# Kernel tuning notes

Measured on AMD Instinct MI355X. Metric: run time of the kernel, lower is better.

The kernel has to match this reference:

```python
import jax, jax.numpy as jnp
import numpy as np

B = 32768   # batch of states (original forward is per-state; we vmap)
D = 3       # coord_dim

_W_SHAPES = [("w_h0",(3,32)),("w_y0",(3,32)),("w_yu0",(3,3)),("w_u0",(3,32)),
             ("w_h1",(32,32)),("w_z1",(32,32)),("w_zu1",(32,32)),("w_y1",(3,32)),
             ("w_yu1",(32,3)),("w_u1",(32,32)),("w_h2",(32,32)),("w_z2",(32,32)),
             ("w_zu2",(32,32)),("w_y2",(3,32)),("w_yu2",(32,3)),("w_u2",(32,32)),
             ("w_z_out",(32,1)),("w_zu_out",(32,32)),("w_y_out",(3,1)),
             ("w_yu_out",(32,3)),("w_u_out",(32,1))]
_B_SHAPES = [("b_y0",(3,)),("b_h0",(32,)),("b_0",(32,)),("b_h1",(32,)),("b_y1",(3,)),
             ("b_z1",(32,)),("b_1",(32,)),("b_h2",(32,)),("b_z2",(32,)),("b_y2",(3,)),
             ("b_2",(32,)),("b_z_out",(32,)),("b_y_out",(3,)),("b_out",(1,))]

def _make_params(key):
    n = len(_W_SHAPES) + len(_B_SHAPES) + 4
    ks = jax.random.split(key, n)
    p, i = {}, 0
    for name, sh in _W_SHAPES:   # torch .uniform_(-0.1, 0.1)
        p[name] = jax.random.uniform(ks[i], sh, jnp.float32, -0.1, 0.1); i += 1
    for name, sh in _B_SHAPES:   # torch.rand -> U[0,1)
        p[name] = jax.random.uniform(ks[i], sh, jnp.float32, 0.0, 1.0); i += 1
    # fc layers: normal init per _init_weights (stds / sqrt(16)=4), zero bias
    stds = [2.2/4.0, 0.58/4.0, 0.58*2.0/4.0, 4.0]
    shapes = [(32, 3), (32, 32), (32, 32), (1, 32)]
    for j in range(4):
        p[f"fc{j+1}_w"] = stds[j] * jax.random.normal(ks[i], shapes[j], jnp.float32); i += 1
        p[f"fc{j+1}_b"] = jnp.zeros((shapes[j][0],), jnp.float32)
    return p

def setup_inputs():
    key = jax.random.key(0)
    kx, kp = jax.random.split(key)
    inp = {"x": jax.random.normal(kx, (B, 2 * D), jnp.float32)}
    inp.update(_make_params(kp))
    return inp

def _forward(x, p):
    sp, relu = jax.nn.softplus, jax.nn.relu

    def lagr(state):
        q, y = state[:D], state[D:]
        u1 = sp(q @ p["w_h0"] + p["b_h0"])
        z1 = sp((y * (q @ p["w_yu0"] + p["b_y0"])) @ p["w_y0"] + q @ p["w_u0"] + p["b_0"])
        u2 = sp(u1 @ p["w_h1"] + p["b_h1"])
        z2 = sp((z1 * (u1 @ p["w_zu1"] + p["b_z1"])) @ relu(p["w_z1"])
                + (y * (u1 @ p["w_yu1"] + p["b_y1"])) @ p["w_y1"]
                + u1 @ p["w_u1"] + p["b_1"])
        u3 = sp(u2 @ p["w_h2"] + p["b_h2"])
        z3 = sp((z2 * (u2 @ p["w_zu2"] + p["b_z2"])) @ relu(p["w_z2"])
                + (y * (u2 @ p["w_yu2"] + p["b_y2"])) @ p["w_y2"]
                + u2 @ p["w_u2"] + p["b_2"])
        zout = sp((z3 * (u3 @ p["w_zu_out"] + p["b_z_out"])) @ relu(p["w_z_out"])
                  + (y * (u3 @ p["w_yu_out"] + p["b_y_out"])) @ p["w_y_out"]
                  + u3 @ p["w_u_out"] + p["b_out"])
        V = sp(q @ p["fc1_w"].T + p["fc1_b"])
        V = sp(V @ p["fc2_w"].T + p["fc2_b"])
        V = sp(V @ p["fc3_w"].T + p["fc3_b"])
        V = V @ p["fc4_w"].T + p["fc4_b"]
        return (zout - V)[0]  # scalar Lagrangian

    def step(state):
        dq = state[D:]
        H = jax.hessian(lagr)(state)        # (6,6)
        g = jax.grad(lagr)(state)[:D]       # dL/dq, matches jacobian row b[0,:3]
        M = H[D:, D:]                       # d2L/ddq ddq
        C = H[D:, :D]                       # d2L/ddq dq
        ddq = (g - dq @ C.T) @ jnp.linalg.inv(M).T
        dx = jnp.concatenate([dq, ddq])
        return state + 0.001 * dx           # Euler step, as in torch forward

    return jax.vmap(step)(x)

def reference(x, w_h0, w_y0, w_yu0, w_u0, w_h1, w_z1, w_zu1, w_y1, w_yu1, w_u1,
              w_h2, w_z2, w_zu2, w_y2, w_yu2, w_u2, w_z_out, w_zu_out, w_y_out,
              w_yu_out, w_u_out, b_y0, b_h0, b_0, b_h1, b_y1, b_z1, b_1, b_h2,
              b_z2, b_y2, b_2, b_z_out, b_y_out, b_out, fc1_w, fc1_b, fc2_w,
              fc2_b, fc3_w, fc3_b, fc4_w, fc4_b):
    p = dict(locals())
    xv = p.pop("x")
    return _forward(xv, p)
```

## Files before the change

### kernel.cpp

```cpp
#include <hip/hip_runtime.h>

#define NTH 64
#define B_TOTAL 32768
#define PSTR 20

typedef float v2f __attribute__((ext_vector_type(2)));
typedef float v4f __attribute__((ext_vector_type(4)));
typedef double v4d __attribute__((ext_vector_type(4)));

struct Ptrs { const float* p[44]; };

enum : int {
  I_X = 0,
  I_WH0 = 1, I_WY0 = 2, I_WYU0 = 3, I_WU0 = 4,
  I_WH1 = 5, I_WZ1 = 6, I_WZU1 = 7, I_WY1 = 8, I_WYU1 = 9, I_WU1 = 10,
  I_WH2 = 11, I_WZ2 = 12, I_WZU2 = 13, I_WY2 = 14, I_WYU2 = 15, I_WU2 = 16,
  I_WZO = 17, I_WZUO = 18, I_WYO = 19, I_WYUO = 20, I_WUO = 21,
  I_BY0 = 22, I_BH0 = 23, I_B0 = 24, I_BH1 = 25, I_BY1 = 26, I_BZ1 = 27, I_B1 = 28,
  I_BH2 = 29, I_BZ2 = 30, I_BY2 = 31, I_B2 = 32, I_BZO = 33, I_BYO = 34, I_BOUT = 35,
  I_FC1 = 36, I_FC1B = 37, I_FC2 = 38, I_FC2B = 39, I_FC3 = 40, I_FC3B = 41,
  I_FC4 = 42, I_FC4B = 43
};

struct V16 { float c[16]; };

__device__ __forceinline__ float spf(float x) {
  return fmaxf(x, 0.0f) + __logf(1.0f + __expf(-fabsf(x)));
}
__device__ __forceinline__ float sigf(float x) {
  return __fdividef(1.0f, 1.0f + __expf(-x));
}

__device__ __forceinline__ V16 spchain16(const V16& A, float y0, float y1, float y2) {
  V16 Z;
  float s = sigf(A.c[0]);
  float d = s * (1.0f - s);
  Z.c[0] = spf(A.c[0]);
#pragma unroll
  for (int a = 0; a < 3; ++a) Z.c[1 + a] = s * A.c[1 + a];
#pragma unroll
  for (int b = 0; b < 3; ++b) Z.c[4 + b] = s * A.c[4 + b];
  Z.c[7]  = s * A.c[7]  + d * A.c[1] * A.c[1];
  Z.c[8]  = s * A.c[8]  + d * A.c[1] * A.c[2];
  Z.c[9]  = s * A.c[9]  + d * A.c[1] * A.c[3];
  Z.c[10] = s * A.c[10] + d * A.c[2] * A.c[2];
  Z.c[11] = s * A.c[11] + d * A.c[2] * A.c[3];
  Z.c[12] = s * A.c[12] + d * A.c[3] * A.c[3];
  float ydq = y0 * A.c[4] + y1 * A.c[5] + y2 * A.c[6];
#pragma unroll
  for (int a = 0; a < 3; ++a) Z.c[13 + a] = s * A.c[13 + a] + d * A.c[1 + a] * ydq;
  return Z;
}

__device__ __forceinline__ void stageProd(float* row, const V16& Z, float S0, float S1,
                                          float S2, float S3, float y0, float y1, float y2) {
  float z0 = Z.c[0];
  float ysd = y0 * S1 + y1 * S2 + y2 * S3;
  v4f w0 = {z0 * S0, S0 * Z.c[1], S0 * Z.c[2], S0 * Z.c[3]};
  v4f w1 = {z0 * S1 + S0 * Z.c[4], z0 * S2 + S0 * Z.c[5], z0 * S3 + S0 * Z.c[6], S0 * Z.c[7]};
  v4f w2 = {S0 * Z.c[8], S0 * Z.c[9], S0 * Z.c[10], S0 * Z.c[11]};
  v4f w3 = {S0 * Z.c[12], S0 * Z.c[13] + Z.c[1] * ysd, S0 * Z.c[14] + Z.c[2] * ysd,
            S0 * Z.c[15] + Z.c[3] * ysd};
  *(v4f*)(row + 0) = w0;  *(v4f*)(row + 4) = w1;
  *(v4f*)(row + 8) = w2;  *(v4f*)(row + 12) = w3;
}

__device__ __forceinline__ V16 prodZS16(const V16& Z, float S0, float S1, float S2, float S3,
                                        float y0, float y1, float y2) {
  V16 P;
  const float Sq[3] = {S1, S2, S3};
  float ysd = y0 * S1 + y1 * S2 + y2 * S3;
  P.c[0] = Z.c[0] * S0;
#pragma unroll
  for (int a = 0; a < 3; ++a) P.c[1 + a] = S0 * Z.c[1 + a];
#pragma unroll
  for (int b = 0; b < 3; ++b) P.c[4 + b] = Z.c[0] * Sq[b] + S0 * Z.c[4 + b];
#pragma unroll
  for (int t = 0; t < 6; ++t) P.c[7 + t] = S0 * Z.c[7 + t];
#pragma unroll
  for (int a = 0; a < 3; ++a) P.c[13 + a] = S0 * Z.c[13 + a] + Z.c[1 + a] * ysd;
  return P;
}

__device__ __forceinline__ void stageU_all(const float* __restrict__ Wh,
                                           const float* __restrict__ Wzu,
                                           const float* __restrict__ Wu,
                                           const float* __restrict__ Wyu, int j,
                                           const float* us,
                                           v2f& h0, v2f& h1, v2f& s0, v2f& s1,
                                           v2f& w0, v2f& w1,
                                           v2f& ta0, v2f& ta1, v2f& tb0, v2f& tb1,
                                           v2f& tc0, v2f& tc1) {
#pragma unroll 2
  for (int i = 0; i < 32; ++i) {
    v4f u = *(const v4f*)(us + i * 4);
    float wh = Wh[i * 32 + j], wz = Wzu[i * 32 + j], wu = Wu[i * 32 + j];
    h0 += u.xy * wh; h1 += u.zw * wh;
    s0 += u.xy * wz; s1 += u.zw * wz;
    w0 += u.xy * wu; w1 += u.zw * wu;
    float wy0 = Wyu[i * 3 + 0], wy1 = Wyu[i * 3 + 1], wy2 = Wyu[i * 3 + 2];
    ta0 += u.xy * wy0; ta1 += u.zw * wy0;
    tb0 += u.xy * wy1; tb1 += u.zw * wy1;
    tc0 += u.xy * wy2; tc1 += u.zw * wy2;
  }
}

__device__ __forceinline__ void buildA16(const float* __restrict__ Wy, int j, float y0, float y1,
                                         float y2, const float wv[4], const float ta[4],
                                         const float tb[4], const float tc[4], V16& A) {
  float wy0 = Wy[j], wy1 = Wy[32 + j], wy2 = Wy[64 + j];
  A.c[0] = wv[0] + y0 * ta[0] * wy0 + y1 * tb[0] * wy1 + y2 * tc[0] * wy2;
  A.c[1] = ta[0] * wy0; A.c[2] = tb[0] * wy1; A.c[3] = tc[0] * wy2;
#pragma unroll
  for (int b = 0; b < 3; ++b)
    A.c[4 + b] = wv[1 + b] + y0 * ta[1 + b] * wy0 + y1 * tb[1 + b] * wy1 + y2 * tc[1 + b] * wy2;
#pragma unroll
  for (int t6 = 0; t6 < 6; ++t6) A.c[7 + t6] = 0.0f;
  float yta = y0 * ta[1] + y1 * ta[2] + y2 * ta[3];
  float ytb = y0 * tb[1] + y1 * tb[2] + y2 * tb[3];
  float ytc = y0 * tc[1] + y1 * tc[2] + y2 * tc[3];
  A.c[13] = yta * wy0; A.c[14] = ytb * wy1; A.c[15] = ytc * wy2;
}

__global__ __launch_bounds__(NTH, 4) void lnn_step_kernel(Ptrs P, float* __restrict__ out) {
  __shared__ float pstage[2][32][PSTR];
  __shared__ float ustage[2][32][4];

  const int tid = threadIdx.x;
  const int j = tid & 31;
  const int half = tid >> 5;
  const int sample = blockIdx.x * 2 + half;

  float* prow = &pstage[half][0][0];
  float* urow = &ustage[half][0][0];
  float* pst0 = &pstage[0][0][0];
  float* pst1 = &pstage[1][0][0];
  const int l64 = tid & 63;
  const int n16 = l64 & 15;
  const int kq = l64 >> 4;

  const float* X = P.p[I_X] + sample * 6;
  const float q0 = X[0], q1 = X[1], q2 = X[2];
  const float y0 = X[3], y1 = X[4], y2 = X[5];

  float Vg0, Vg1, Vg2;
  {
    const float* fc1 = P.p[I_FC1];
    float f0 = fc1[j * 3], f1 = fc1[j * 3 + 1], f2 = fc1[j * 3 + 2];
    float hp = P.p[I_FC1B][j] + q0 * f0 + q1 * f1 + q2 * f2;
    float ss = sigf(hp);
    *(v4f*)(urow + j * 4) = (v4f){spf(hp), ss * f0, ss * f1, ss * f2};
    const float* fc2 = P.p[I_FC2] + j * 32;
    v2f a0 = {P.p[I_FC2B][j], 0.0f}, a1 = {0.0f, 0.0f};
#pragma unroll 2
    for (int r = 0; r < 8; ++r) {
      v4f w4 = *(const v4f*)(fc2 + r * 4);
      v4f u0 = *(const v4f*)(urow + (r * 4 + 0) * 4);
      v4f u1 = *(const v4f*)(urow + (r * 4 + 1) * 4);
      v4f u2 = *(const v4f*)(urow + (r * 4 + 2) * 4);
      v4f u3 = *(const v4f*)(urow + (r * 4 + 3) * 4);
      a0 += u0.xy * w4.x; a1 += u0.zw * w4.x;
      a0 += u1.xy * w4.y; a1 += u1.zw * w4.y;
      a0 += u2.xy * w4.z; a1 += u2.zw * w4.z;
      a0 += u3.xy * w4.w; a1 += u3.zw * w4.w;
    }
    float ss2 = sigf(a0.x);
    *(v4f*)(urow + j * 4) = (v4f){spf(a0.x), ss2 * a0.y, ss2 * a1.x, ss2 * a1.y};
    const float* fc3 = P.p[I_FC3] + j * 32;
    v2f b0 = {P.p[I_FC3B][j], 0.0f}, b1 = {0.0f, 0.0f};
#pragma unroll 2
    for (int r = 0; r < 8; ++r) {
      v4f w4 = *(const v4f*)(fc3 + r * 4);
      v4f u0 = *(const v4f*)(urow + (r * 4 + 0) * 4);
      v4f u1 = *(const v4f*)(urow + (r * 4 + 1) * 4);
      v4f u2 = *(const v4f*)(urow + (r * 4 + 2) * 4);
      v4f u3 = *(const v4f*)(urow + (r * 4 + 3) * 4);
      b0 += u0.xy * w4.x; b1 += u0.zw * w4.x;
      b0 += u1.xy * w4.y; b1 += u1.zw * w4.y;
      b0 += u2.xy * w4.z; b1 += u2.zw * w4.z;
      b0 += u3.xy * w4.w; b1 += u3.zw * w4.w;
    }
    float ss3 = sigf(b0.x);
    float f4 = P.p[I_FC4][j];
    Vg0 = ss3 * b0.y * f4; Vg1 = ss3 * b1.x * f4; Vg2 = ss3 * b1.y * f4;
  }

  const float* yu0 = P.p[I_WYU0];
  float t0v[3];
#pragma unroll
  for (int k = 0; k < 3; ++k)
    t0v[k] = q0 * yu0[k] + q1 * yu0[3 + k] + q2 * yu0[6 + k] + P.p[I_BY0][k];

  float u1c[4];
  {
    const float* wh0 = P.p[I_WH0];
    float w0 = wh0[j], w1 = wh0[32 + j], w2 = wh0[64 + j];
    float h = P.p[I_BH0][j] + q0 * w0 + q1 * w1 + q2 * w2;
    float ss = sigf(h);
    u1c[0] = spf(h); u1c[1] = ss * w0; u1c[2] = ss * w1; u1c[3] = ss * w2;
  }

  V16 z;
  {
    const float* Wy = P.p[I_WY0];
    const float* Wu = P.p[I_WU0];
    float wy0 = Wy[j], wy1 = Wy[32 + j], wy2 = Wy[64 + j];
    float wu0 = Wu[j], wu1 = Wu[32 + j], wu2 = Wu[64 + j];
    V16 A;
    A.c[0] = P.p[I_B0][j] + (y0 * t0v[0]) * wy0 + (y1 * t0v[1]) * wy1 + (y2 * t0v[2]) * wy2 +
             q0 * wu0 + q1 * wu1 + q2 * wu2;
    A.c[1] = t0v[0] * wy0; A.c[2] = t0v[1] * wy1; A.c[3] = t0v[2] * wy2;
#pragma unroll
    for (int b = 0; b < 3; ++b) {
      float acc = (b == 0 ? wu0 : (b == 1 ? wu1 : wu2));
      acc += y0 * yu0[b * 3 + 0] * wy0 + y1 * yu0[b * 3 + 1] * wy1 + y2 * yu0[b * 3 + 2] * wy2;
      A.c[4 + b] = acc;
    }
#pragma unroll
    for (int t = 0; t < 6; ++t) A.c[7 + t] = 0.0f;
    float yty0 = y0 * yu0[0] + y1 * yu0[3] + y2 * yu0[6];
    float yty1 = y0 * yu0[1] + y1 * yu0[4] + y2 * yu0[7];
    float yty2 = y0 * yu0[2] + y1 * yu0[5] + y2 * yu0[8];
    A.c[13] = yty0 * wy0; A.c[14] = yty1 * wy1; A.c[15] = yty2 * wy2;
    z = spchain16(A, y0, y1, y2);
  }

  float unext[4];
#pragma unroll 1
  for (int lvl = 0; lvl < 2; ++lvl) {
    const float* Wh  = P.p[lvl == 0 ? I_WH1 : I_WH2];
    const float* Wzu = P.p[lvl == 0 ? I_WZU1 : I_WZU2];
    const float* Wu  = P.p[lvl == 0 ? I_WU1 : I_WU2];
    const float* Wyu = P.p[lvl == 0 ? I_WYU1 : I_WYU2];
    const float* Wy  = P.p[lvl == 0 ? I_WY1 : I_WY2];
    const float* Wz  = P.p[lvl == 0 ? I_WZ1 : I_WZ2];
    const float* Bh  = P.p[lvl == 0 ? I_BH1 : I_BH2];
    const float* Bz  = P.p[lvl == 0 ? I_BZ1 : I_BZ2];
    const float* Bl  = P.p[lvl == 0 ? I_B1 : I_B2];
    const float* By  = P.p[lvl == 0 ? I_BY1 : I_BY2];

    const float* uc = (lvl == 0) ? u1c : unext;
    *(v4f*)(urow + j * 4) = (v4f){uc[0], uc[1], uc[2], uc[3]};

    v2f h0 = {Bh[j], 0.0f}, h1 = {0.0f, 0.0f};
    v2f s0 = {Bz[j], 0.0f}, s1 = {0.0f, 0.0f};
    v2f w0 = {Bl[j], 0.0f}, w1 = {0.0f, 0.0f};
    v2f ta0 = {By[0], 0.0f}, ta1 = {0.0f, 0.0f};
    v2f tb0 = {By[1], 0.0f}, tb1 = {0.0f, 0.0f};
    v2f tc0 = {By[2], 0.0f}, tc1 = {0.0f, 0.0f};
    stageU_all(Wh, Wzu, Wu, Wyu, j, urow, h0, h1, s0, s1, w0, w1,
               ta0, ta1, tb0, tb1, tc0, tc1);
    {
      float ss = sigf(h0.x);
      unext[0] = spf(h0.x); unext[1] = ss * h0.y; unext[2] = ss * h1.x; unext[3] = ss * h1.y;
    }
    stageProd(prow + j * PSTR, z, s0.x, s0.y, s1.x, s1.y, y0, y1, y2);

    v4d a00 = {0.0, 0.0, 0.0, 0.0};
    v4d a01 = {0.0, 0.0, 0.0, 0.0};
    v4d a10 = {0.0, 0.0, 0.0, 0.0};
    v4d a11 = {0.0, 0.0, 0.0, 0.0};
#pragma unroll
    for (int c = 0; c < 8; ++c) {
      const int i = c * 4 + kq;
      double b0 = (double)pst0[i * PSTR + n16];
      double b1 = (double)pst1[i * PSTR + n16];
      double wlo = (double)fmaxf(Wz[i * 32 + n16], 0.0f);
      double whi = (double)fmaxf(Wz[i * 32 + 16 + n16], 0.0f);
      a00 = __builtin_amdgcn_mfma_f64_16x16x4f64(wlo, b0, a00, 0, 0, 0);
      a01 = __builtin_amdgcn_mfma_f64_16x16x4f64(whi, b0, a01, 0, 0, 0);
      a10 = __builtin_amdgcn_mfma_f64_16x16x4f64(wlo, b1, a10, 0, 0, 0);
      a11 = __builtin_amdgcn_mfma_f64_16x16x4f64(whi, b1, a11, 0, 0, 0);
    }
#pragma unroll
    for (int r = 0; r < 4; ++r) {
      pst0[(kq + 4 * r) * PSTR + n16]        = (float)a00[r];
      pst0[(16 + kq + 4 * r) * PSTR + n16]   = (float)a01[r];
      pst1[(kq + 4 * r) * PSTR + n16]        = (float)a10[r];
      pst1[(16 + kq + 4 * r) * PSTR + n16]   = (float)a11[r];
    }

    float wvv[4] = {w0.x, w0.y, w1.x, w1.y};
    float tav[4] = {ta0.x, ta0.y, ta1.x, ta1.y};
    float tbv[4] = {tb0.x, tb0.y, tb1.x, tb1.y};
    float tcv[4] = {tc0.x, tc0.y, tc1.x, tc1.y};
    V16 A2;
    buildA16(Wy, j, y0, y1, y2, wvv, tav, tbv, tcv, A2);

    {
      const float* rown = prow + j * PSTR;
      v4f r0 = *(const v4f*)(rown + 0);
      v4f r1 = *(const v4f*)(rown + 4);
      v4f r2 = *(const v4f*)(rown + 8);
      v4f r3 = *(const v4f*)(rown + 12);
      A2.c[0] += r0.x;  A2.c[1] += r0.y;  A2.c[2] += r0.z;  A2.c[3] += r0.w;
      A2.c[4] += r1.x;  A2.c[5] += r1.y;  A2.c[6] += r1.z;  A2.c[7] += r1.w;
      A2.c[8] += r2.x;  A2.c[9] += r2.y;  A2.c[10] += r2.z; A2.c[11] += r2.w;
      A2.c[12] += r3.x; A2.c[13] += r3.y; A2.c[14] += r3.z; A2.c[15] += r3.w;
    }
    z = spchain16(A2, y0, y1, y2);
  }

  *(v4f*)(urow + j * 4) = (v4f){unext[0], unext[1], unext[2], unext[3]};
  v2f s30 = {P.p[I_BZO][j], 0.0f}, s31 = {0.0f, 0.0f};
  v2f wo0 = {0.0f, 0.0f}, wo1 = {0.0f, 0.0f};
  v2f t3a0 = {P.p[I_BYO][0], 0.0f}, t3a1 = {0.0f, 0.0f};
  v2f t3b0 = {P.p[I_BYO][1], 0.0f}, t3b1 = {0.0f, 0.0f};
  v2f t3c0 = {P.p[I_BYO][2], 0.0f}, t3c1 = {0.0f, 0.0f};
  {
    const float* Wzuo = P.p[I_WZUO];
    const float* Wuo = P.p[I_WUO];
    const float* Wyuo = P.p[I_WYUO];
#pragma unroll 2
    for (int i = 0; i < 32; ++i) {
      v4f u = *(const v4f*)(urow + i * 4);
      float wz = Wzuo[i * 32 + j];
      s30 += u.xy * wz; s31 += u.zw * wz;
      float wu = Wuo[i];
      wo0 += u.xy * wu; wo1 += u.zw * wu;
      float wy0 = Wyuo[i * 3], wy1 = Wyuo[i * 3 + 1], wy2 = Wyuo[i * 3 + 2];
      t3a0 += u.xy * wy0; t3a1 += u.zw * wy0;
      t3b0 += u.xy * wy1; t3b1 += u.zw * wy1;
      t3c0 += u.xy * wy2; t3c1 += u.zw * wy2;
    }
  }
  const float woc[4] = {wo0.x, wo0.y, wo1.x, wo1.y};
  const float t3av[4] = {t3a0.x, t3a0.y, t3a1.x, t3a1.y};
  const float t3bv[4] = {t3b0.x, t3b0.y, t3b1.x, t3b1.y};
  const float t3cv[4] = {t3c0.x, t3c0.y, t3c1.x, t3c1.y};

  float red[19];
  {
    V16 p3 = prodZS16(z, s30.x, s30.y, s31.x, s31.y, y0, y1, y2);
    float wz = fmaxf(P.p[I_WZO][j], 0.0f);
#pragma unroll
    for (int k = 0; k < 16; ++k) red[k] = p3.c[k] * wz;
    red[16] = Vg0; red[17] = Vg1; red[18] = Vg2;
  }
#pragma unroll
  for (int m = 16; m >= 1; m >>= 1) {
#pragma unroll
    for (int k = 0; k < 19; ++k) red[k] += __shfl_xor(red[k], m, 32);
  }

  if (j == 0) {
    const float* Wyo = P.p[I_WYO];
    const float wyo0 = Wyo[0], wyo1 = Wyo[1], wyo2 = Wyo[2];
    float Av = red[0] + woc[0] + P.p[I_BOUT][0] + y0 * t3av[0] * wyo0 +
               y1 * t3bv[0] * wyo1 + y2 * t3cv[0] * wyo2;
    float Agy[3];
    Agy[0] = red[1] + t3av[0] * wyo0;
    Agy[1] = red[2] + t3bv[0] * wyo1;
    Agy[2] = red[3] + t3cv[0] * wyo2;
    float Agq[3];
#pragma unroll
    for (int b = 0; b < 3; ++b)
      Agq[b] = red[4 + b] + woc[1 + b] + y0 * t3av[1 + b] * wyo0 +
               y1 * t3bv[1 + b] * wyo1 + y2 * t3cv[1 + b] * wyo2;
    float ycq[3];
    ycq[0] = red[13] + (y0 * t3av[1] + y1 * t3av[2] + y2 * t3av[3]) * wyo0;
    ycq[1] = red[14] + (y0 * t3bv[1] + y1 * t3bv[2] + y2 * t3bv[3]) * wyo1;
    ycq[2] = red[15] + (y0 * t3cv[1] + y1 * t3cv[2] + y2 * t3cv[3]) * wyo2;
    float s = sigf(Av), d = s * (1.0f - s);

    double Mm[3][3];
    const int pa[6] = {0, 0, 0, 1, 1, 2}, pb[6] = {0, 1, 2, 1, 2, 2};
#pragma unroll
    for (int t = 0; t < 6; ++t) {
      double m = (double)s * (double)red[7 + t] +
                 (double)d * (double)Agy[pa[t]] * (double)Agy[pb[t]];
      Mm[pa[t]][pb[t]] = m; Mm[pb[t]][pa[t]] = m;
    }
    double yAgq = (double)y0 * (double)Agq[0] + (double)y1 * (double)Agq[1] +
                  (double)y2 * (double)Agq[2];
    double rr[3];
#pragma unroll
    for (int a = 0; a < 3; ++a) {
      double g = (double)s * (double)Agq[a] - (double)red[16 + a];
      double Cy = (double)s * (double)ycq[a] + (double)d * (double)Agy[a] * yAgq;
      rr[a] = g - Cy;
    }
    double a = Mm[0][0], b_ = Mm[0][1], c_ = Mm[0][2], dd = Mm[1][1], e = Mm[1][2], f = Mm[2][2];
    double A00 = dd * f - e * e, A01 = c_ * e - b_ * f, A02 = b_ * e - c_ * dd;
    double A11 = a * f - c_ * c_, A12 = b_ * c_ - a * e, A22 = a * dd - b_ * b_;
    double det = a * A00 + b_ * A01 + c_ * A02;
    double idet = 1.0 / det;
    double d0 = (A00 * rr[0] + A01 * rr[1] + A02 * rr[2]) * idet;
    double d1 = (A01 * rr[0] + A11 * rr[1] + A12 * rr[2]) * idet;
    double d2 = (A02 * rr[0] + A12 * rr[1] + A22 * rr[2]) * idet;

    float* O = out + (size_t)sample * 6;
    O[0] = q0 + 0.001f * y0;
    O[1] = q1 + 0.001f * y1;
    O[2] = q2 + 0.001f * y2;
    O[3] = y0 + 0.001f * (float)d0;
    O[4] = y1 + 0.001f * (float)d1;
    O[5] = y2 + 0.001f * (float)d2;
  }
}

extern "C" void kernel_launch(void* const* d_in, const int* in_sizes, int n_in,
                              void* d_out, int out_size, void* d_ws, size_t ws_size,
                              hipStream_t stream) {
  (void)in_sizes; (void)n_in; (void)d_ws; (void)ws_size; (void)out_size;
  Ptrs P;
  for (int i = 0; i < 44; ++i) P.p[i] = (const float*)d_in[i];
  float* out = (float*)d_out;
  dim3 grid(B_TOTAL / 2), block(NTH);
  hipLaunchKernelGGL(lnn_step_kernel, grid, block, 0, stream, P, out);
}
```

Before: 130.6 us.

## Compute per-level u-matrix-vector products with f64 MFMA through shared scratch

Replaces the scalar per-thread loops that multiply the 4-wide u tangent vectors by Wh, Wzu, Wu, Wyu and the output-layer weights with double-precision 16x16x4 MFMA calls. Results are staged through new shared scratch buffers and read back per lane. This is meant to move FMA work off the vector ALU. In exchange it adds many shared-memory round trips and serialized matrix ops, and mostly-zero padded MFMAs for the 3-column Wyu products. It also relies on wavefront-synchronous LDS ordering with no explicit barriers.

```diff
diff --git a/kernel.cpp b/kernel.cpp
--- a/kernel.cpp
+++ b/kernel.cpp
@@ -82,29 +82,6 @@
   return P;
 }
 
-__device__ __forceinline__ void stageU_all(const float* __restrict__ Wh,
-                                           const float* __restrict__ Wzu,
-                                           const float* __restrict__ Wu,
-                                           const float* __restrict__ Wyu, int j,
-                                           const float* us,
-                                           v2f& h0, v2f& h1, v2f& s0, v2f& s1,
-                                           v2f& w0, v2f& w1,
-                                           v2f& ta0, v2f& ta1, v2f& tb0, v2f& tb1,
-                                           v2f& tc0, v2f& tc1) {
-#pragma unroll 2
-  for (int i = 0; i < 32; ++i) {
-    v4f u = *(const v4f*)(us + i * 4);
-    float wh = Wh[i * 32 + j], wz = Wzu[i * 32 + j], wu = Wu[i * 32 + j];
-    h0 += u.xy * wh; h1 += u.zw * wh;
-    s0 += u.xy * wz; s1 += u.zw * wz;
-    w0 += u.xy * wu; w1 += u.zw * wu;
-    float wy0 = Wyu[i * 3 + 0], wy1 = Wyu[i * 3 + 1], wy2 = Wyu[i * 3 + 2];
-    ta0 += u.xy * wy0; ta1 += u.zw * wy0;
-    tb0 += u.xy * wy1; tb1 += u.zw * wy1;
-    tc0 += u.xy * wy2; tc1 += u.zw * wy2;
-  }
-}
-
 __device__ __forceinline__ void buildA16(const float* __restrict__ Wy, int j, float y0, float y1,
                                          float y2, const float wv[4], const float ta[4],
                                          const float tb[4], const float tc[4], V16& A) {
@@ -122,9 +99,44 @@
   A.c[13] = yta * wy0; A.c[14] = ytb * wy1; A.c[15] = ytc * wy2;
 }
 
+__device__ __forceinline__ void mfmaMV32(const float* __restrict__ W,
+                                         const float* ub, int n16, int kq, float* scrW) {
+  v4d a0 = {0.0, 0.0, 0.0, 0.0}, a1 = {0.0, 0.0, 0.0, 0.0};
+#pragma unroll
+  for (int c = 0; c < 8; ++c) {
+    const int i = c * 4 + kq;
+    double b = (double)ub[i * 4];
+    a0 = __builtin_amdgcn_mfma_f64_16x16x4f64((double)W[i * 32 + n16], b, a0, 0, 0, 0);
+    a1 = __builtin_amdgcn_mfma_f64_16x16x4f64((double)W[i * 32 + 16 + n16], b, a1, 0, 0, 0);
+  }
+#pragma unroll
+  for (int r = 0; r < 4; ++r) {
+    scrW[(kq + 4 * r) * PSTR + n16]      = (float)a0[r];
+    scrW[(16 + kq + 4 * r) * PSTR + n16] = (float)a1[r];
+  }
+}
+
+__device__ __forceinline__ void mfmaMV4(const float* __restrict__ Wyu,
+                                        const float* __restrict__ Wrow3,
+                                        const float* ub, int n16, int kq, float* cscr) {
+  v4d a = {0.0, 0.0, 0.0, 0.0};
+#pragma unroll
+  for (int c = 0; c < 8; ++c) {
+    const int i = c * 4 + kq;
+    double b = (double)ub[i * 4];
+    double av = 0.0;
+    if (n16 < 3) av = (double)Wyu[i * 3 + n16];
+    else if (n16 == 3 && Wrow3) av = (double)Wrow3[i];
+    a = __builtin_amdgcn_mfma_f64_16x16x4f64(av, b, a, 0, 0, 0);
+  }
+  cscr[kq * 16 + n16] = (float)a[0];
+}
+
 __global__ __launch_bounds__(NTH, 4) void lnn_step_kernel(Ptrs P, float* __restrict__ out) {
   __shared__ float pstage[2][32][PSTR];
   __shared__ float ustage[2][32][4];
+  __shared__ float scrW[32][PSTR];
+  __shared__ float cscr[4][16];
 
   const int tid = threadIdx.x;
   const int j = tid & 31;
@@ -135,9 +147,12 @@
   float* urow = &ustage[half][0][0];
   float* pst0 = &pstage[0][0][0];
   float* pst1 = &pstage[1][0][0];
+  float* scw = &scrW[0][0];
+  float* csc = &cscr[0][0];
   const int l64 = tid & 63;
   const int n16 = l64 & 15;
   const int kq = l64 >> 4;
+  const float* ubase = &ustage[(n16 >> 2) & 1][0][0] + (n16 & 3);
 
   const float* X = P.p[I_X] + sample * 6;
   const float q0 = X[0], q1 = X[1], q2 = X[2];
@@ -242,19 +257,31 @@
     const float* uc = (lvl == 0) ? u1c : unext;
     *(v4f*)(urow + j * 4) = (v4f){uc[0], uc[1], uc[2], uc[3]};
 
-    v2f h0 = {Bh[j], 0.0f}, h1 = {0.0f, 0.0f};
-    v2f s0 = {Bz[j], 0.0f}, s1 = {0.0f, 0.0f};
-    v2f w0 = {Bl[j], 0.0f}, w1 = {0.0f, 0.0f};
-    v2f ta0 = {By[0], 0.0f}, ta1 = {0.0f, 0.0f};
-    v2f tb0 = {By[1], 0.0f}, tb1 = {0.0f, 0.0f};
-    v2f tc0 = {By[2], 0.0f}, tc1 = {0.0f, 0.0f};
-    stageU_all(Wh, Wzu, Wu, Wyu, j, urow, h0, h1, s0, s1, w0, w1,
-               ta0, ta1, tb0, tb1, tc0, tc1);
+    mfmaMV32(Wh, ubase, n16, kq, scw);
     {
-      float ss = sigf(h0.x);
-      unext[0] = spf(h0.x); unext[1] = ss * h0.y; unext[2] = ss * h1.x; unext[3] = ss * h1.y;
-    }
-    stageProd(prow + j * PSTR, z, s0.x, s0.y, s1.x, s1.y, y0, y1, y2);
+      v4f hv = *(const v4f*)(scw + j * PSTR + half * 4);
+      float hb = Bh[j] + hv.x;
+      float ssh = sigf(hb);
+      unext[0] = spf(hb); unext[1] = ssh * hv.y; unext[2] = ssh * hv.z; unext[3] = ssh * hv.w;
+    }
+    mfmaMV32(Wzu, ubase, n16, kq, scw);
+    {
+      v4f sv = *(const v4f*)(scw + j * PSTR + half * 4);
+      stageProd(prow + j * PSTR, z, Bz[j] + sv.x, sv.y, sv.z, sv.w, y0, y1, y2);
+    }
+    mfmaMV32(Wu, ubase, n16, kq, scw);
+    v4f wv4 = *(const v4f*)(scw + j * PSTR + half * 4);
+    mfmaMV4(Wyu, nullptr, ubase, n16, kq, csc);
+    v4f t0r = *(const v4f*)(csc + 0 * 16 + half * 4);
+    v4f t1r = *(const v4f*)(csc + 1 * 16 + half * 4);
+    v4f t2r = *(const v4f*)(csc + 2 * 16 + half * 4);
+
+    float wvv[4] = {Bl[j] + wv4.x, wv4.y, wv4.z, wv4.w};
+    float tav[4] = {By[0] + t0r.x, t0r.y, t0r.z, t0r.w};
+    float tbv[4] = {By[1] + t1r.x, t1r.y, t1r.z, t1r.w};
+    float tcv[4] = {By[2] + t2r.x, t2r.y, t2r.z, t2r.w};
+    V16 A2;
+    buildA16(Wy, j, y0, y1, y2, wvv, tav, tbv, tcv, A2);
 
     v4d a00 = {0.0, 0.0, 0.0, 0.0};
     v4d a01 = {0.0, 0.0, 0.0, 0.0};
@@ -280,13 +307,6 @@
       pst1[(16 + kq + 4 * r) * PSTR + n16]   = (float)a11[r];
     }
 
-    float wvv[4] = {w0.x, w0.y, w1.x, w1.y};
-    float tav[4] = {ta0.x, ta0.y, ta1.x, ta1.y};
-    float tbv[4] = {tb0.x, tb0.y, tb1.x, tb1.y};
-    float tcv[4] = {tc0.x, tc0.y, tc1.x, tc1.y};
-    V16 A2;
-    buildA16(Wy, j, y0, y1, y2, wvv, tav, tbv, tcv, A2);
-
     {
       const float* rown = prow + j * PSTR;
       v4f r0 = *(const v4f*)(rown + 0);
@@ -302,36 +322,22 @@
   }
 
   *(v4f*)(urow + j * 4) = (v4f){unext[0], unext[1], unext[2], unext[3]};
-  v2f s30 = {P.p[I_BZO][j], 0.0f}, s31 = {0.0f, 0.0f};
-  v2f wo0 = {0.0f, 0.0f}, wo1 = {0.0f, 0.0f};
-  v2f t3a0 = {P.p[I_BYO][0], 0.0f}, t3a1 = {0.0f, 0.0f};
-  v2f t3b0 = {P.p[I_BYO][1], 0.0f}, t3b1 = {0.0f, 0.0f};
-  v2f t3c0 = {P.p[I_BYO][2], 0.0f}, t3c1 = {0.0f, 0.0f};
-  {
-    const float* Wzuo = P.p[I_WZUO];
-    const float* Wuo = P.p[I_WUO];
-    const float* Wyuo = P.p[I_WYUO];
-#pragma unroll 2
-    for (int i = 0; i < 32; ++i) {
-      v4f u = *(const v4f*)(urow + i * 4);
-      float wz = Wzuo[i * 32 + j];
-      s30 += u.xy * wz; s31 += u.zw * wz;
-      float wu = Wuo[i];
-      wo0 += u.xy * wu; wo1 += u.zw * wu;
-      float wy0 = Wyuo[i * 3], wy1 = Wyuo[i * 3 + 1], wy2 = Wyuo[i * 3 + 2];
-      t3a0 += u.xy * wy0; t3a1 += u.zw * wy0;
-      t3b0 += u.xy * wy1; t3b1 += u.zw * wy1;
-      t3c0 += u.xy * wy2; t3c1 += u.zw * wy2;
-    }
-  }
-  const float woc[4] = {wo0.x, wo0.y, wo1.x, wo1.y};
-  const float t3av[4] = {t3a0.x, t3a0.y, t3a1.x, t3a1.y};
-  const float t3bv[4] = {t3b0.x, t3b0.y, t3b1.x, t3b1.y};
-  const float t3cv[4] = {t3c0.x, t3c0.y, t3c1.x, t3c1.y};
+  mfmaMV32(P.p[I_WZUO], ubase, n16, kq, scw);
+  v4f s3v = *(const v4f*)(scw + j * PSTR + half * 4);
+  mfmaMV4(P.p[I_WYUO], P.p[I_WUO], ubase, n16, kq, csc);
+  v4f t3r0 = *(const v4f*)(csc + 0 * 16 + half * 4);
+  v4f t3r1 = *(const v4f*)(csc + 1 * 16 + half * 4);
+  v4f t3r2 = *(const v4f*)(csc + 2 * 16 + half * 4);
+  v4f wor  = *(const v4f*)(csc + 3 * 16 + half * 4);
+  const float woc[4]  = {wor.x, wor.y, wor.z, wor.w};
+  const float t3av[4] = {P.p[I_BYO][0] + t3r0.x, t3r0.y, t3r0.z, t3r0.w};
+  const float t3bv[4] = {P.p[I_BYO][1] + t3r1.x, t3r1.y, t3r1.z, t3r1.w};
+  const float t3cv[4] = {P.p[I_BYO][2] + t3r2.x, t3r2.y, t3r2.z, t3r2.w};
+  const float s3c[4]  = {P.p[I_BZO][j] + s3v.x, s3v.y, s3v.z, s3v.w};
 
   float red[19];
   {
-    V16 p3 = prodZS16(z, s30.x, s30.y, s31.x, s31.y, y0, y1, y2);
+    V16 p3 = prodZS16(z, s3c[0], s3c[1], s3c[2], s3c[3], y0, y1, y2);
     float wz = fmaxf(P.p[I_WZO][j], 0.0f);
 #pragma unroll
     for (int k = 0; k < 16; ++k) red[k] = p3.c[k] * wz;
```

Measured after the change: 243.3 us. 86.3% more time.
